# Kernel optimization log

Measured on AMD Instinct MI355X. Metric: run time of the kernel, lower is better.

The kernel has to match this reference:

```python
import jax, jax.numpy as jnp
import numpy as np

N_NODES = 100000
N_GRAPHS = 512


def gcn_conv(x, W, b, src, dst, n_nodes):
    """PyG GCNConv: out = D^{-1/2} (A + I) D^{-1/2} (x W) + b, scatter at dst."""
    xw = x @ W  # [N, out_dim]
    # add self loops
    loop = jnp.arange(n_nodes, dtype=src.dtype)
    src_f = jnp.concatenate([src, loop])
    dst_f = jnp.concatenate([dst, loop])
    # symmetric normalization: deg from unit edge weights on dst
    deg = jax.ops.segment_sum(jnp.ones_like(dst_f, dtype=xw.dtype), dst_f,
                              num_segments=n_nodes)
    dinv = jnp.where(deg > 0, jax.lax.rsqrt(deg), 0.0)
    norm = dinv[src_f] * dinv[dst_f]  # [E+N]
    msg = xw[src_f] * norm[:, None]   # gather + scale, [E+N, out_dim]
    out = jax.ops.segment_sum(msg, dst_f, num_segments=n_nodes)
    return out + b


def global_mean_pool(x, batch, num_graphs):
    s = jax.ops.segment_sum(x, batch, num_segments=num_graphs)
    cnt = jax.ops.segment_sum(jnp.ones((x.shape[0],), x.dtype), batch,
                              num_segments=num_graphs)
    return s / jnp.maximum(cnt, 1.0)[:, None]


def setup_inputs() -> dict:
    key = jax.random.key(0)
    ks = jax.random.split(key, 10)
    d_in, h1, h2, d_out = 128, 128, 128, 32
    n_edges = 1600000
    x = jax.random.normal(ks[0], (N_NODES, d_in), dtype=jnp.float32)
    edge_index = jax.random.randint(ks[1], (2, n_edges), 0, N_NODES, dtype=jnp.int64)
    batch = jnp.sort(jax.random.randint(ks[2], (N_NODES,), 0, N_GRAPHS, dtype=jnp.int64))
    s1 = 1.0 / np.sqrt(d_in)
    s2 = 1.0 / np.sqrt(h1)
    s3 = 1.0 / np.sqrt(h2)
    W1 = jax.random.uniform(ks[3], (d_in, h1), jnp.float32, -s1, s1)
    b1 = jnp.zeros((h1,), jnp.float32)
    W2 = jax.random.uniform(ks[4], (h1, h2), jnp.float32, -s2, s2)
    b2 = jnp.zeros((h2,), jnp.float32)
    Wl = jax.random.uniform(ks[5], (h2, d_out), jnp.float32, -s3 * np.sqrt(6.0), s3 * np.sqrt(6.0))
    bl = jax.random.uniform(ks[6], (d_out,), jnp.float32, -s3, s3)
    return {"x": x, "edge_index": edge_index, "batch": batch,
            "W1": W1, "b1": b1, "W2": W2, "b2": b2, "Wl": Wl, "bl": bl}


def reference(x, edge_index, batch, W1, b1, W2, b2, Wl, bl):
    src, dst = edge_index[0], edge_index[1]
    h = gcn_conv(x, W1, b1, src, dst, N_NODES)
    h = jax.nn.relu(h)
    h = gcn_conv(h, W2, b2, src, dst, N_NODES)
    g = global_mean_pool(h, batch, N_GRAPHS)
    g = jax.nn.relu(g)
    return g @ Wl + bl
```

## Files before the change

### kernel.cpp

```cpp
#include <hip/hip_runtime.h>
#include <hip/hip_fp16.h>

#define DIM 128
#define NGRAPH 512
#define BUCKET_SHIFT 9
#define BUCKET_NODES 512

__device__ __forceinline__ int edge_at(const int* p, long long idx, int is64) {
  return is64 ? p[idx * 2] : p[(size_t)idx];
}

__global__ void k_detect(const int* __restrict__ ei, int* __restrict__ flag) {
  if (threadIdx.x == 0) {
    int all0 = 1;
    for (int k = 0; k < 32; ++k)
      if (ei[2 * k + 1] != 0) all0 = 0;
    *flag = all0;
  }
}

__global__ __launch_bounds__(256) void k_bucket_hist(const int* __restrict__ ei, int E,
                                                     const int* __restrict__ flag,
                                                     int* __restrict__ bucket_count,
                                                     int nbuck) {
  __shared__ int h[256];
  int tid = threadIdx.x;
  h[tid] = 0;
  __syncthreads();
  int is64 = *flag;
  int half = E >> 1;
  if (is64) {
    const int4* dp = (const int4*)(ei + 2 * (size_t)E);
    for (int t = blockIdx.x * 256 + tid; t < half; t += gridDim.x * 256) {
      int4 d = dp[t];
      atomicAdd(&h[d.x >> BUCKET_SHIFT], 1);
      atomicAdd(&h[d.z >> BUCKET_SHIFT], 1);
    }
  } else {
    const int2* dp = (const int2*)(ei + (size_t)E);
    for (int t = blockIdx.x * 256 + tid; t < half; t += gridDim.x * 256) {
      int2 d = dp[t];
      atomicAdd(&h[d.x >> BUCKET_SHIFT], 1);
      atomicAdd(&h[d.y >> BUCKET_SHIFT], 1);
    }
  }
  __syncthreads();
  if (tid < nbuck && h[tid]) atomicAdd(&bucket_count[tid], h[tid]);
  if ((E & 1) && blockIdx.x == 0 && tid == 0) {
    int d = edge_at(ei, (long long)E + (E - 1), is64);
    atomicAdd(&bucket_count[d >> BUCKET_SHIFT], 1);
  }
}

__global__ __launch_bounds__(256) void k_bucket_scan(const int* __restrict__ bucket_count,
                                                     int* __restrict__ bucket_off,
                                                     int* __restrict__ bucket_cursor,
                                                     int* __restrict__ row_off,
                                                     int nbuck, int N, int E) {
  __shared__ int s[256];
  int t = threadIdx.x;
  int v = (t < nbuck) ? bucket_count[t] : 0;
  s[t] = v;
  __syncthreads();
  for (int off = 1; off < 256; off <<= 1) {
    int u = (t >= off) ? s[t - off] : 0;
    __syncthreads();
    s[t] += u;
    __syncthreads();
  }
  int excl = s[t] - v;
  if (t < nbuck) { bucket_off[t] = excl; bucket_cursor[t] = excl; }
  if (t == 0) { bucket_off[nbuck] = E; row_off[N] = E; }
}

__global__ __launch_bounds__(256) void k_scatter(const int* __restrict__ ei, int E,
                                                 const int* __restrict__ flag,
                                                 int* __restrict__ bucket_cursor,
                                                 int2* __restrict__ staging, int nbuck) {
  __shared__ int h[256];
  __shared__ int basebuf[256];
  int tid = threadIdx.x;
  int half = E >> 1;
  int ppb = (half + gridDim.x - 1) / gridDim.x;
  int lo = blockIdx.x * ppb;
  int hi = min(lo + ppb, half);
  h[tid] = 0;
  __syncthreads();
  int is64 = *flag;
  if (is64) {
    const int4* dp = (const int4*)(ei + 2 * (size_t)E);
    for (int t = lo + tid; t < hi; t += 256) {
      int4 d = dp[t];
      atomicAdd(&h[d.x >> BUCKET_SHIFT], 1);
      atomicAdd(&h[d.z >> BUCKET_SHIFT], 1);
    }
  } else {
    const int2* dp = (const int2*)(ei + (size_t)E);
    for (int t = lo + tid; t < hi; t += 256) {
      int2 d = dp[t];
      atomicAdd(&h[d.x >> BUCKET_SHIFT], 1);
      atomicAdd(&h[d.y >> BUCKET_SHIFT], 1);
    }
  }
  __syncthreads();
  if (tid < nbuck) {
    int c = h[tid];
    if (c) basebuf[tid] = atomicAdd(&bucket_cursor[tid], c);
    h[tid] = 0;
  }
  __syncthreads();
  if (is64) {
    const int4* sp = (const int4*)ei;
    const int4* dp = (const int4*)(ei + 2 * (size_t)E);
    for (int t = lo + tid; t < hi; t += 256) {
      int4 sv = sp[t];
      int4 dv = dp[t];
      int b0 = dv.x >> BUCKET_SHIFT;
      int l0 = atomicAdd(&h[b0], 1);
      staging[basebuf[b0] + l0] = make_int2(sv.x, dv.x);
      int b1 = dv.z >> BUCKET_SHIFT;
      int l1 = atomicAdd(&h[b1], 1);
      staging[basebuf[b1] + l1] = make_int2(sv.z, dv.z);
    }
  } else {
    const int2* sp = (const int2*)ei;
    const int2* dp = (const int2*)(ei + (size_t)E);
    for (int t = lo + tid; t < hi; t += 256) {
      int2 sv = sp[t];
      int2 dv = dp[t];
      int b0 = dv.x >> BUCKET_SHIFT;
      int l0 = atomicAdd(&h[b0], 1);
      staging[basebuf[b0] + l0] = make_int2(sv.x, dv.x);
      int b1 = dv.y >> BUCKET_SHIFT;
      int l1 = atomicAdd(&h[b1], 1);
      staging[basebuf[b1] + l1] = make_int2(sv.y, dv.y);
    }
  }
  if ((E & 1) && blockIdx.x == 0 && tid == 0) {
    int s0 = edge_at(ei, E - 1, is64);
    int d0 = edge_at(ei, (long long)E + (E - 1), is64);
    int pos = atomicAdd(&bucket_cursor[d0 >> BUCKET_SHIFT], 1);
    staging[pos] = make_int2(s0, d0);
  }
}

__global__ __launch_bounds__(256) void k_csr_build(const int2* __restrict__ staging,
                                                   const int* __restrict__ bucket_off,
                                                   int* __restrict__ row_off,
                                                   float* __restrict__ dinv,
                                                   int* __restrict__ csr_src, int N) {
  __shared__ int cnt_s[BUCKET_NODES];
  __shared__ int s[256];
  int tid = threadIdx.x;
  int b = blockIdx.x;
  int base = b << BUCKET_SHIFT;
  cnt_s[tid] = 0;
  cnt_s[tid + 256] = 0;
  __syncthreads();
  int start = bucket_off[b], end = bucket_off[b + 1];
  for (int i = start + tid; i < end; i += 256) {
    int2 e = staging[i];
    atomicAdd(&cnt_s[e.y - base], 1);
  }
  __syncthreads();
  int a0 = cnt_s[2 * tid], a1 = cnt_s[2 * tid + 1];
  int ps = a0 + a1;
  s[tid] = ps;
  __syncthreads();
  for (int off = 1; off < 256; off <<= 1) {
    int u = (tid >= off) ? s[tid - off] : 0;
    __syncthreads();
    s[tid] += u;
    __syncthreads();
  }
  int excl = s[tid] - ps;
  int r0 = start + excl;
  int r1 = r0 + a0;
  cnt_s[2 * tid] = r0;
  cnt_s[2 * tid + 1] = r1;
  int n0 = base + 2 * tid, n1 = n0 + 1;
  if (n0 < N) { row_off[n0] = r0; dinv[n0] = rsqrtf((float)(a0 + 1)); }
  if (n1 < N) { row_off[n1] = r1; dinv[n1] = rsqrtf((float)(a1 + 1)); }
  __syncthreads();
  for (int i = start + tid; i < end; i += 256) {
    int2 e = staging[i];
    int pos = atomicAdd(&cnt_s[e.y - base], 1);
    csr_src[pos] = e.x;
  }
}

__global__ __launch_bounds__(256) void k_gemm128(const float* __restrict__ A,
                                                 const float* __restrict__ W,
                                                 const float* __restrict__ dinv,
                                                 __half* __restrict__ Y, int M) {
  __shared__ float sA[16][64];
  __shared__ float sB[16][128];
  int tid = threadIdx.x;
  int m0 = blockIdx.x * 64;
  int tm = tid >> 5;
  int tc = tid & 31;
  float acc[8][4];
#pragma unroll
  for (int m = 0; m < 8; ++m)
#pragma unroll
    for (int c = 0; c < 4; ++c) acc[m][c] = 0.f;

  int lr = tid >> 2;
  int lk = (tid & 3) * 4;
  int ar = m0 + lr; if (ar >= M) ar = M - 1;
  int br = tid >> 5;
  int bc = (tid & 31) * 4;

  for (int k0 = 0; k0 < 128; k0 += 16) {
    float4 va = *(const float4*)&A[(size_t)ar * 128 + k0 + lk];
    sA[lk + 0][lr] = va.x; sA[lk + 1][lr] = va.y;
    sA[lk + 2][lr] = va.z; sA[lk + 3][lr] = va.w;
    *(float4*)&sB[br][bc]     = *(const float4*)&W[(k0 + br) * 128 + bc];
    *(float4*)&sB[br + 8][bc] = *(const float4*)&W[(k0 + br + 8) * 128 + bc];
    __syncthreads();
#pragma unroll
    for (int kk = 0; kk < 16; ++kk) {
      float4 a0 = *(const float4*)&sA[kk][tm * 8];
      float4 a1 = *(const float4*)&sA[kk][tm * 8 + 4];
      float4 bq = *(const float4*)&sB[kk][tc * 4];
      float av[8] = {a0.x, a0.y, a0.z, a0.w, a1.x, a1.y, a1.z, a1.w};
      float bv[4] = {bq.x, bq.y, bq.z, bq.w};
#pragma unroll
      for (int m = 0; m < 8; ++m)
#pragma unroll
        for (int c = 0; c < 4; ++c) acc[m][c] += av[m] * bv[c];
    }
    __syncthreads();
  }
#pragma unroll
  for (int m = 0; m < 8; ++m) {
    int row = m0 + tm * 8 + m;
    if (row < M) {
      float dr = dinv[row];
      __half2 h0 = __floats2half2_rn(acc[m][0] * dr, acc[m][1] * dr);
      __half2 h1 = __floats2half2_rn(acc[m][2] * dr, acc[m][3] * dr);
      __half2* yp = (__half2*)&Y[(size_t)row * 128 + tc * 4];
      yp[0] = h0; yp[1] = h1;
    }
  }
}

__global__ __launch_bounds__(256) void k_aggregate(
    const __half* __restrict__ y, const int* __restrict__ csr_src,
    const int* __restrict__ row_off, const float* __restrict__ dinv,
    const float* __restrict__ bias, float* __restrict__ out, int do_relu, int N) {
  int node = blockIdx.x * 4 + (threadIdx.x >> 6);
  if (node >= N) return;
  int lane = threadIdx.x & 63;
  int beg = row_off[node], end = row_off[node + 1];
  float di = dinv[node];
  const __half2* base = (const __half2*)y;
  __half2 sv = base[(size_t)node * 64 + lane];
  float ax = __low2float(sv), ay = __high2float(sv);
  int e = beg;
  for (; e + 8 <= end; e += 8) {
    int s0 = csr_src[e + 0], s1 = csr_src[e + 1], s2 = csr_src[e + 2], s3 = csr_src[e + 3];
    int s4 = csr_src[e + 4], s5 = csr_src[e + 5], s6 = csr_src[e + 6], s7 = csr_src[e + 7];
    __half2 v0 = base[(size_t)s0 * 64 + lane];
    __half2 v1 = base[(size_t)s1 * 64 + lane];
    __half2 v2 = base[(size_t)s2 * 64 + lane];
    __half2 v3 = base[(size_t)s3 * 64 + lane];
    __half2 v4 = base[(size_t)s4 * 64 + lane];
    __half2 v5 = base[(size_t)s5 * 64 + lane];
    __half2 v6 = base[(size_t)s6 * 64 + lane];
    __half2 v7 = base[(size_t)s7 * 64 + lane];
    ax += __low2float(v0); ay += __high2float(v0);
    ax += __low2float(v1); ay += __high2float(v1);
    ax += __low2float(v2); ay += __high2float(v2);
    ax += __low2float(v3); ay += __high2float(v3);
    ax += __low2float(v4); ay += __high2float(v4);
    ax += __low2float(v5); ay += __high2float(v5);
    ax += __low2float(v6); ay += __high2float(v6);
    ax += __low2float(v7); ay += __high2float(v7);
  }
  for (; e < end; ++e) {
    __half2 v0 = base[(size_t)csr_src[e] * 64 + lane];
    ax += __low2float(v0); ay += __high2float(v0);
  }
  float2 b = ((const float2*)bias)[lane];
  ax = di * ax + b.x;
  ay = di * ay + b.y;
  if (do_relu) { ax = fmaxf(ax, 0.f); ay = fmaxf(ay, 0.f); }
  float2 o; o.x = ax; o.y = ay;
  ((float2*)out)[(size_t)node * 64 + lane] = o;
}

__device__ __forceinline__ int batch_at(const int* b, int i, int is64) {
  return is64 ? b[i * 2] : b[i];
}

__global__ __launch_bounds__(128) void k_pool(const float* __restrict__ h,
                                              const int* __restrict__ batch,
                                              float* __restrict__ g, int n,
                                              const int* __restrict__ flag) {
  int gid = blockIdx.x;
  int is64 = *flag;
  __shared__ int bounds[2];
  if (threadIdx.x < 2) {
    int target = gid + threadIdx.x;
    int lo = 0, hi = n;
    while (lo < hi) {
      int mid = (lo + hi) >> 1;
      if (batch_at(batch, mid, is64) < target) lo = mid + 1; else hi = mid;
    }
    bounds[threadIdx.x] = lo;
  }
  __syncthreads();
  int lo = bounds[0], hi = bounds[1];
  float s = 0.f;
  for (int r = lo; r < hi; ++r) s += h[(size_t)r * 128 + threadIdx.x];
  float c = (float)(hi - lo);
  float m = s / fmaxf(c, 1.0f);
  g[gid * 128 + threadIdx.x] = fmaxf(m, 0.f);
}

__global__ __launch_bounds__(256) void k_final(const float* __restrict__ g,
                                               const float* __restrict__ Wl,
                                               const float* __restrict__ bl,
                                               float* __restrict__ out) {
  __shared__ float sW[128 * 32];
  for (int t = threadIdx.x; t < 128 * 32; t += 256) sW[t] = Wl[t];
  __syncthreads();
  int r = blockIdx.x * 8 + (threadIdx.x >> 5);
  int c = threadIdx.x & 31;
  const float* gr = &g[r * 128];
  float acc = bl[c];
#pragma unroll 4
  for (int k = 0; k < 128; ++k) acc += gr[k] * sW[k * 32 + c];
  out[r * 32 + c] = acc;
}

extern "C" void kernel_launch(void* const* d_in, const int* in_sizes, int n_in,
                              void* d_out, int out_size, void* d_ws, size_t ws_size,
                              hipStream_t stream) {
  const float* x   = (const float*)d_in[0];
  const int* ei    = (const int*)d_in[1];
  const int* batch = (const int*)d_in[2];
  const float* W1  = (const float*)d_in[3];
  const float* b1  = (const float*)d_in[4];
  const float* W2  = (const float*)d_in[5];
  const float* b2  = (const float*)d_in[6];
  const float* Wl  = (const float*)d_in[7];
  const float* bl  = (const float*)d_in[8];
  float* out = (float*)d_out;

  const int N = in_sizes[0] / DIM;
  const int E = in_sizes[1] / 2;
  const int NBUCK = (N + BUCKET_NODES - 1) >> BUCKET_SHIFT;

  size_t need = (size_t)N * DIM * 2
              + (size_t)N * DIM * 4
              + (size_t)E * 4
              + (size_t)(N + 1) * 4
              + (size_t)N * 4
              + 3 * 1088 + 64
              + (size_t)NGRAPH * DIM * 4;
  if (ws_size < need) return;

  char* w = (char*)d_ws;
  __half* bufY  = (__half*)w; w += (size_t)N * DIM * 2;
  float* bufH   = (float*)w;  w += (size_t)N * DIM * 4;
  int* csr_src  = (int*)w;    w += (size_t)E * 4;
  int* row_off  = (int*)w;    w += (size_t)(N + 1) * 4;
  float* dinv   = (float*)w;  w += (size_t)N * 4;
  int* bucket_count  = (int*)w; w += 1088;
  int* bucket_off    = (int*)w; w += 1088;
  int* bucket_cursor = (int*)w; w += 1088;
  int* flag     = (int*)w;    w += 64;
  float* pooled = (float*)w;  w += (size_t)NGRAPH * DIM * 4;
  int2* staging = (int2*)bufY;

  hipMemsetAsync(bucket_count, 0, 1088, stream);
  k_detect<<<1, 64, 0, stream>>>(ei, flag);
  k_bucket_hist<<<1024, 256, 0, stream>>>(ei, E, flag, bucket_count, NBUCK);
  k_bucket_scan<<<1, 256, 0, stream>>>(bucket_count, bucket_off, bucket_cursor,
                                       row_off, NBUCK, N, E);
  k_scatter<<<1024, 256, 0, stream>>>(ei, E, flag, bucket_cursor, staging, NBUCK);
  k_csr_build<<<NBUCK, 256, 0, stream>>>(staging, bucket_off, row_off, dinv, csr_src, N);

  k_gemm128<<<(N + 63) / 64, 256, 0, stream>>>(x, W1, dinv, bufY, N);
  k_aggregate<<<(N + 3) / 4, 256, 0, stream>>>(bufY, csr_src, row_off, dinv, b1, bufH, 1, N);
  k_gemm128<<<(N + 63) / 64, 256, 0, stream>>>(bufH, W2, dinv, bufY, N);
  k_aggregate<<<(N + 3) / 4, 256, 0, stream>>>(bufY, csr_src, row_off, dinv, b2, bufH, 0, N);
  k_pool<<<NGRAPH, 128, 0, stream>>>(bufH, batch, pooled, N, flag);
  k_final<<<NGRAPH / 8, 256, 0, stream>>>(pooled, Wl, bl, out);
}
```

Measured before the change: 517.2 us.

## Use split-fp16 MFMA GEMM, stage CSR indices in LDS, fuse pool and final

The scalar fp32 GEMM is replaced with an MFMA 16x16x32 fp16 kernel. Both A and W are split into high and low halves, and three MFMAs per tile keep accuracy close to fp32. The aggregate kernel now preloads each block's CSR source indices into shared memory before the gathers. Pooling and the final linear layer are fused into one kernel, and the detect kernel is folded into the histogram and scatter kernels, which saves launches. The split-fp16 scheme costs three MFMAs per tile and converts W once per block, and the aggregate kernel gains an extra sync and shared-memory footprint.

```diff
diff --git a/kernel.cpp b/kernel.cpp
--- a/kernel.cpp
+++ b/kernel.cpp
@@ -6,28 +6,28 @@
 #define BUCKET_SHIFT 9
 #define BUCKET_NODES 512
 
+typedef _Float16 half8 __attribute__((ext_vector_type(8)));
+typedef float floatx4 __attribute__((ext_vector_type(4)));
+
+__device__ __forceinline__ int detect64(const int* __restrict__ ei) {
+  int all0 = 1;
+#pragma unroll
+  for (int k = 0; k < 32; ++k) all0 &= (ei[2 * k + 1] == 0);
+  return all0;
+}
+
 __device__ __forceinline__ int edge_at(const int* p, long long idx, int is64) {
   return is64 ? p[idx * 2] : p[(size_t)idx];
 }
 
-__global__ void k_detect(const int* __restrict__ ei, int* __restrict__ flag) {
-  if (threadIdx.x == 0) {
-    int all0 = 1;
-    for (int k = 0; k < 32; ++k)
-      if (ei[2 * k + 1] != 0) all0 = 0;
-    *flag = all0;
-  }
-}
-
 __global__ __launch_bounds__(256) void k_bucket_hist(const int* __restrict__ ei, int E,
-                                                     const int* __restrict__ flag,
                                                      int* __restrict__ bucket_count,
                                                      int nbuck) {
   __shared__ int h[256];
   int tid = threadIdx.x;
   h[tid] = 0;
   __syncthreads();
-  int is64 = *flag;
+  int is64 = detect64(ei);
   int half = E >> 1;
   if (is64) {
     const int4* dp = (const int4*)(ei + 2 * (size_t)E);
@@ -74,7 +74,7 @@
 }
 
 __global__ __launch_bounds__(256) void k_scatter(const int* __restrict__ ei, int E,
-                                                 const int* __restrict__ flag,
+                                                 int* __restrict__ flag,
                                                  int* __restrict__ bucket_cursor,
                                                  int2* __restrict__ staging, int nbuck) {
   __shared__ int h[256];
@@ -86,7 +86,8 @@
   int hi = min(lo + ppb, half);
   h[tid] = 0;
   __syncthreads();
-  int is64 = *flag;
+  int is64 = detect64(ei);
+  if (blockIdx.x == 0 && tid == 0) *flag = is64;
   if (is64) {
     const int4* dp = (const int4*)(ei + 2 * (size_t)E);
     for (int t = lo + tid; t < hi; t += 256) {
@@ -189,59 +190,82 @@
   }
 }
 
-__global__ __launch_bounds__(256) void k_gemm128(const float* __restrict__ A,
-                                                 const float* __restrict__ W,
-                                                 const float* __restrict__ dinv,
-                                                 __half* __restrict__ Y, int M) {
-  __shared__ float sA[16][64];
-  __shared__ float sB[16][128];
-  int tid = threadIdx.x;
-  int m0 = blockIdx.x * 64;
-  int tm = tid >> 5;
-  int tc = tid & 31;
-  float acc[8][4];
-#pragma unroll
-  for (int m = 0; m < 8; ++m)
-#pragma unroll
-    for (int c = 0; c < 4; ++c) acc[m][c] = 0.f;
-
-  int lr = tid >> 2;
-  int lk = (tid & 3) * 4;
-  int ar = m0 + lr; if (ar >= M) ar = M - 1;
-  int br = tid >> 5;
-  int bc = (tid & 31) * 4;
-
-  for (int k0 = 0; k0 < 128; k0 += 16) {
-    float4 va = *(const float4*)&A[(size_t)ar * 128 + k0 + lk];
-    sA[lk + 0][lr] = va.x; sA[lk + 1][lr] = va.y;
-    sA[lk + 2][lr] = va.z; sA[lk + 3][lr] = va.w;
-    *(float4*)&sB[br][bc]     = *(const float4*)&W[(k0 + br) * 128 + bc];
-    *(float4*)&sB[br + 8][bc] = *(const float4*)&W[(k0 + br + 8) * 128 + bc];
-    __syncthreads();
-#pragma unroll
-    for (int kk = 0; kk < 16; ++kk) {
-      float4 a0 = *(const float4*)&sA[kk][tm * 8];
-      float4 a1 = *(const float4*)&sA[kk][tm * 8 + 4];
-      float4 bq = *(const float4*)&sB[kk][tc * 4];
-      float av[8] = {a0.x, a0.y, a0.z, a0.w, a1.x, a1.y, a1.z, a1.w};
-      float bv[4] = {bq.x, bq.y, bq.z, bq.w};
-#pragma unroll
-      for (int m = 0; m < 8; ++m)
-#pragma unroll
-        for (int c = 0; c < 4; ++c) acc[m][c] += av[m] * bv[c];
-    }
-    __syncthreads();
-  }
-#pragma unroll
-  for (int m = 0; m < 8; ++m) {
-    int row = m0 + tm * 8 + m;
-    if (row < M) {
-      float dr = dinv[row];
-      __half2 h0 = __floats2half2_rn(acc[m][0] * dr, acc[m][1] * dr);
-      __half2 h1 = __floats2half2_rn(acc[m][2] * dr, acc[m][3] * dr);
-      __half2* yp = (__half2*)&Y[(size_t)row * 128 + tc * 4];
-      yp[0] = h0; yp[1] = h1;
-    }
+__global__ __launch_bounds__(256) void k_gemm_mfma(
+    const float* __restrict__ A, const float* __restrict__ W,
+    const float* __restrict__ dinv, __half* __restrict__ Y, int M) {
+  __shared__ _Float16 WH[16384];
+  __shared__ _Float16 WL[16384];
+  __shared__ _Float16 OT[4][16 * 128];
+  int tid = threadIdx.x;
+
+  for (int idx = tid; idx < 2048; idx += 256) {
+    int l = idx & 63, c = (idx >> 6) & 7, s = idx >> 9;
+    int kbase = s * 32 + ((l >> 4) << 3);
+    int col = c * 16 + (l & 15);
+#pragma unroll
+    for (int j = 0; j < 8; ++j) {
+      float w = W[(kbase + j) * 128 + col];
+      _Float16 hh = (_Float16)w;
+      WH[idx * 8 + j] = hh;
+      WL[idx * 8 + j] = (_Float16)(w - (float)hh);
+    }
+  }
+  __syncthreads();
+
+  int wid = tid >> 6, l = tid & 63;
+  int row0 = blockIdx.x * 64 + wid * 16;
+  int arow = row0 + (l & 15);
+  if (arow >= M) arow = M - 1;
+
+  floatx4 acc[8];
+#pragma unroll
+  for (int c = 0; c < 8; ++c) acc[c] = (floatx4){0.f, 0.f, 0.f, 0.f};
+
+#pragma unroll
+  for (int s = 0; s < 4; ++s) {
+    const float* ap = &A[(size_t)arow * 128 + s * 32 + ((l >> 4) << 3)];
+    float4 f0 = *(const float4*)ap;
+    float4 f1 = *(const float4*)(ap + 4);
+    float fv[8] = {f0.x, f0.y, f0.z, f0.w, f1.x, f1.y, f1.z, f1.w};
+    half8 ah, alo;
+#pragma unroll
+    for (int j = 0; j < 8; ++j) {
+      _Float16 hh = (_Float16)fv[j];
+      ah[j] = hh;
+      alo[j] = (_Float16)(fv[j] - (float)hh);
+    }
+#pragma unroll
+    for (int c = 0; c < 8; ++c) {
+      int fi = ((s * 8 + c) * 64 + l) * 8;
+      half8 bh = *(half8*)&WH[fi];
+      half8 bl8 = *(half8*)&WL[fi];
+      acc[c] = __builtin_amdgcn_mfma_f32_16x16x32_f16(ah, bh, acc[c], 0, 0, 0);
+      acc[c] = __builtin_amdgcn_mfma_f32_16x16x32_f16(alo, bh, acc[c], 0, 0, 0);
+      acc[c] = __builtin_amdgcn_mfma_f32_16x16x32_f16(ah, bl8, acc[c], 0, 0, 0);
+    }
+  }
+
+  _Float16* ot = &OT[wid][0];
+  int lrb = (l >> 4) * 4;
+  float dv[4];
+#pragma unroll
+  for (int r = 0; r < 4; ++r) {
+    int gr = row0 + lrb + r;
+    dv[r] = (gr < M) ? dinv[gr] : 0.f;
+  }
+#pragma unroll
+  for (int c = 0; c < 8; ++c)
+#pragma unroll
+    for (int r = 0; r < 4; ++r)
+      ot[(lrb + r) * 128 + c * 16 + (l & 15)] = (_Float16)(acc[c][r] * dv[r]);
+  const float4* otf = (const float4*)ot;
+#pragma unroll
+  for (int q = 0; q < 4; ++q) {
+    int idx = q * 64 + l;
+    int lrow = idx >> 4;
+    int coff = (idx & 15) * 8;
+    int grow = row0 + lrow;
+    if (grow < M) *(float4*)&Y[(size_t)grow * 128 + coff] = otf[idx];
   }
 }
 
@@ -249,38 +273,45 @@
     const __half* __restrict__ y, const int* __restrict__ csr_src,
     const int* __restrict__ row_off, const float* __restrict__ dinv,
     const float* __restrict__ bias, float* __restrict__ out, int do_relu, int N) {
-  int node = blockIdx.x * 4 + (threadIdx.x >> 6);
+  __shared__ int sidx[1024];
+  int tid = threadIdx.x;
+  int n0 = blockIdx.x * 4;
+  int lastn = min(n0 + 4, N);
+  int blockBeg = row_off[n0];
+  int blockEnd = row_off[lastn];
+  int len = blockEnd - blockBeg;
+  int nload = min(len, 1024);
+  for (int t = tid; t < nload; t += 256) sidx[t] = csr_src[blockBeg + t];
+  __syncthreads();
+  int node = n0 + (tid >> 6);
   if (node >= N) return;
-  int lane = threadIdx.x & 63;
+  int lane = tid & 63;
   int beg = row_off[node], end = row_off[node + 1];
   float di = dinv[node];
   const __half2* base = (const __half2*)y;
   __half2 sv = base[(size_t)node * 64 + lane];
   float ax = __low2float(sv), ay = __high2float(sv);
   int e = beg;
-  for (; e + 8 <= end; e += 8) {
-    int s0 = csr_src[e + 0], s1 = csr_src[e + 1], s2 = csr_src[e + 2], s3 = csr_src[e + 3];
-    int s4 = csr_src[e + 4], s5 = csr_src[e + 5], s6 = csr_src[e + 6], s7 = csr_src[e + 7];
-    __half2 v0 = base[(size_t)s0 * 64 + lane];
-    __half2 v1 = base[(size_t)s1 * 64 + lane];
-    __half2 v2 = base[(size_t)s2 * 64 + lane];
-    __half2 v3 = base[(size_t)s3 * 64 + lane];
-    __half2 v4 = base[(size_t)s4 * 64 + lane];
-    __half2 v5 = base[(size_t)s5 * 64 + lane];
-    __half2 v6 = base[(size_t)s6 * 64 + lane];
-    __half2 v7 = base[(size_t)s7 * 64 + lane];
-    ax += __low2float(v0); ay += __high2float(v0);
-    ax += __low2float(v1); ay += __high2float(v1);
-    ax += __low2float(v2); ay += __high2float(v2);
-    ax += __low2float(v3); ay += __high2float(v3);
-    ax += __low2float(v4); ay += __high2float(v4);
-    ax += __low2float(v5); ay += __high2float(v5);
-    ax += __low2float(v6); ay += __high2float(v6);
-    ax += __low2float(v7); ay += __high2float(v7);
-  }
-  for (; e < end; ++e) {
-    __half2 v0 = base[(size_t)csr_src[e] * 64 + lane];
-    ax += __low2float(v0); ay += __high2float(v0);
+  if (len <= nload) {
+    for (; e + 8 <= end; e += 8) {
+      int idx[8];
+#pragma unroll
+      for (int j = 0; j < 8; ++j) idx[j] = sidx[e - blockBeg + j];
+      __half2 v[8];
+#pragma unroll
+      for (int j = 0; j < 8; ++j) v[j] = base[(size_t)idx[j] * 64 + lane];
+#pragma unroll
+      for (int j = 0; j < 8; ++j) { ax += __low2float(v[j]); ay += __high2float(v[j]); }
+    }
+    for (; e < end; ++e) {
+      __half2 v0 = base[(size_t)sidx[e - blockBeg] * 64 + lane];
+      ax += __low2float(v0); ay += __high2float(v0);
+    }
+  } else {
+    for (; e < end; ++e) {
+      __half2 v0 = base[(size_t)csr_src[e] * 64 + lane];
+      ax += __low2float(v0); ay += __high2float(v0);
+    }
   }
   float2 b = ((const float2*)bias)[lane];
   ax = di * ax + b.x;
@@ -290,49 +321,39 @@
   ((float2*)out)[(size_t)node * 64 + lane] = o;
 }
 
-__device__ __forceinline__ int batch_at(const int* b, int i, int is64) {
-  return is64 ? b[i * 2] : b[i];
-}
-
-__global__ __launch_bounds__(128) void k_pool(const float* __restrict__ h,
-                                              const int* __restrict__ batch,
-                                              float* __restrict__ g, int n,
-                                              const int* __restrict__ flag) {
+__global__ __launch_bounds__(128) void k_pool_final(
+    const float* __restrict__ h, const int* __restrict__ batch,
+    const float* __restrict__ Wl, const float* __restrict__ bl,
+    float* __restrict__ out, int n, const int* __restrict__ flag) {
+  __shared__ float sW[128 * 32];
+  __shared__ float sg[128];
+  __shared__ int bounds[2];
+  int tid = threadIdx.x;
   int gid = blockIdx.x;
+  for (int t = tid; t < 128 * 32; t += 128) sW[t] = Wl[t];
   int is64 = *flag;
-  __shared__ int bounds[2];
-  if (threadIdx.x < 2) {
-    int target = gid + threadIdx.x;
+  if (tid < 2) {
+    int target = gid + tid;
     int lo = 0, hi = n;
     while (lo < hi) {
       int mid = (lo + hi) >> 1;
-      if (batch_at(batch, mid, is64) < target) lo = mid + 1; else hi = mid;
-    }
-    bounds[threadIdx.x] = lo;
+      int bv = is64 ? batch[2 * mid] : batch[mid];
+      if (bv < target) lo = mid + 1; else hi = mid;
+    }
+    bounds[tid] = lo;
   }
   __syncthreads();
   int lo = bounds[0], hi = bounds[1];
   float s = 0.f;
-  for (int r = lo; r < hi; ++r) s += h[(size_t)r * 128 + threadIdx.x];
-  float c = (float)(hi - lo);
-  float m = s / fmaxf(c, 1.0f);
-  g[gid * 128 + threadIdx.x] = fmaxf(m, 0.f);
-}
-
-__global__ __launch_bounds__(256) void k_final(const float* __restrict__ g,
-                                               const float* __restrict__ Wl,
-                                               const float* __restrict__ bl,
-                                               float* __restrict__ out) {
-  __shared__ float sW[128 * 32];
-  for (int t = threadIdx.x; t < 128 * 32; t += 256) sW[t] = Wl[t];
-  __syncthreads();
-  int r = blockIdx.x * 8 + (threadIdx.x >> 5);
-  int c = threadIdx.x & 31;
-  const float* gr = &g[r * 128];
-  float acc = bl[c];
-#pragma unroll 4
-  for (int k = 0; k < 128; ++k) acc += gr[k] * sW[k * 32 + c];
-  out[r * 32 + c] = acc;
+  for (int r = lo; r < hi; ++r) s += h[(size_t)r * 128 + tid];
+  sg[tid] = fmaxf(s / fmaxf((float)(hi - lo), 1.f), 0.f);
+  __syncthreads();
+  if (tid < 32) {
+    float acc = bl[tid];
+#pragma unroll 8
+    for (int k = 0; k < 128; ++k) acc += sg[k] * sW[k * 32 + tid];
+    out[gid * 32 + tid] = acc;
+  }
 }
 
 extern "C" void kernel_launch(void* const* d_in, const int* in_sizes, int n_in,
@@ -353,13 +374,8 @@
   const int E = in_sizes[1] / 2;
   const int NBUCK = (N + BUCKET_NODES - 1) >> BUCKET_SHIFT;
 
-  size_t need = (size_t)N * DIM * 2
-              + (size_t)N * DIM * 4
-              + (size_t)E * 4
-              + (size_t)(N + 1) * 4
-              + (size_t)N * 4
-              + 3 * 1088 + 64
-              + (size_t)NGRAPH * DIM * 4;
+  size_t need = (size_t)N * DIM * 2 + (size_t)N * DIM * 4 + (size_t)E * 4
+              + (size_t)(N + 1) * 4 + (size_t)N * 4 + 3 * 1088 + 64;
   if (ws_size < need) return;
 
   char* w = (char*)d_ws;
@@ -372,21 +388,18 @@
   int* bucket_off    = (int*)w; w += 1088;
   int* bucket_cursor = (int*)w; w += 1088;
   int* flag     = (int*)w;    w += 64;
-  float* pooled = (float*)w;  w += (size_t)NGRAPH * DIM * 4;
   int2* staging = (int2*)bufY;
 
   hipMemsetAsync(bucket_count, 0, 1088, stream);
-  k_detect<<<1, 64, 0, stream>>>(ei, flag);
-  k_bucket_hist<<<1024, 256, 0, stream>>>(ei, E, flag, bucket_count, NBUCK);
+  k_bucket_hist<<<1024, 256, 0, stream>>>(ei, E, bucket_count, NBUCK);
   k_bucket_scan<<<1, 256, 0, stream>>>(bucket_count, bucket_off, bucket_cursor,
                                        row_off, NBUCK, N, E);
   k_scatter<<<1024, 256, 0, stream>>>(ei, E, flag, bucket_cursor, staging, NBUCK);
   k_csr_build<<<NBUCK, 256, 0, stream>>>(staging, bucket_off, row_off, dinv, csr_src, N);
 
-  k_gemm128<<<(N + 63) / 64, 256, 0, stream>>>(x, W1, dinv, bufY, N);
+  k_gemm_mfma<<<(N + 63) / 64, 256, 0, stream>>>(x, W1, dinv, bufY, N);
   k_aggregate<<<(N + 3) / 4, 256, 0, stream>>>(bufY, csr_src, row_off, dinv, b1, bufH, 1, N);
-  k_gemm128<<<(N + 63) / 64, 256, 0, stream>>>(bufH, W2, dinv, bufY, N);
+  k_gemm_mfma<<<(N + 63) / 64, 256, 0, stream>>>(bufH, W2, dinv, bufY, N);
   k_aggregate<<<(N + 3) / 4, 256, 0, stream>>>(bufY, csr_src, row_off, dinv, b2, bufH, 0, N);
-  k_pool<<<NGRAPH, 128, 0, stream>>>(bufH, batch, pooled, N, flag);
-  k_final<<<NGRAPH / 8, 256, 0, stream>>>(pooled, Wl, bl, out);
-}
+  k_pool_final<<<NGRAPH, 128, 0, stream>>>(bufH, batch, Wl, bl, out, N, flag);
+}
```

New measurement: 459.2 us. 11.2% less time.
